# Kernel tuning notes

Hardware: AMD Instinct MI355X
Metric: run time of the kernel (lower is better)

## Reference

```python
import jax, jax.numpy as jnp
import numpy as np

B, L, HS = 2, 2048, 2048
NH, NKV, HD = 16, 4, 128
EPS = 1e-6
ROPE_BASE = 10000.0
SCALE = HD ** -0.5


def setup_inputs() -> dict:
    key = jax.random.key(0)
    ks = jax.random.split(key, 5)
    w = lambda k, shape: (jax.random.normal(k, shape, jnp.float32) * 0.02)
    return {
        "hidden_states": jax.random.normal(ks[0], (B, L, HS), jnp.float32),
        "Wq": w(ks[1], (HS, NH * HD)),
        "Wk": w(ks[2], (HS, NKV * HD)),
        "Wv": w(ks[3], (HS, NKV * HD)),
        "Wo": w(ks[4], (NH * HD, HS)),
        "q_norm_w": jnp.ones((HD,), jnp.float32),
        "k_norm_w": jnp.ones((HD,), jnp.float32),
    }


def _rmsnorm(x, w):
    return x * jax.lax.rsqrt(jnp.mean(x * x, axis=-1, keepdims=True) + EPS) * w


def _rope(x, cos, sin):
    # x: [B, L, heads, HD]; cos/sin: [1, L, 1, HD//2]
    x1, x2 = jnp.split(x, 2, axis=-1)
    return jnp.concatenate([x1 * cos - x2 * sin, x2 * cos + x1 * sin], axis=-1)


def reference(hidden_states, Wq, Wk, Wv, Wo, q_norm_w, k_norm_w):
    b, l, _ = hidden_states.shape
    n_rep = NH // NKV
    q = (hidden_states @ Wq).reshape(b, l, NH, HD)
    k = (hidden_states @ Wk).reshape(b, l, NKV, HD)
    v = (hidden_states @ Wv).reshape(b, l, NKV, HD)
    # QK RMSNorm over head_dim
    q = _rmsnorm(q, q_norm_w)
    k = _rmsnorm(k, k_norm_w)
    # RoPE with position_ids = arange(L)
    pos = jnp.arange(l, dtype=jnp.float32)
    inv_freq = 1.0 / (ROPE_BASE ** (jnp.arange(0, HD, 2, dtype=jnp.float32) / HD))
    ang = pos[:, None] * inv_freq  # [L, HD//2]
    cos = jnp.cos(ang)[None, :, None, :]
    sin = jnp.sin(ang)[None, :, None, :]
    q = _rope(q, cos, sin)
    k = _rope(k, cos, sin)
    # GQA: torch expand+reshape gives q head h -> kv head (h mod NKV);
    # reshape q to [B, L, n_rep, NKV, HD] (h = r*NKV + j) and contract per kv group.
    qg = q.reshape(b, l, n_rep, NKV, HD)
    scores = jnp.einsum("blrjd,bmjd->brjlm", qg, k) * SCALE  # [B, r, j, L, L]
    causal = jnp.tril(jnp.ones((l, l), dtype=bool))
    scores = jnp.where(causal, scores, -jnp.inf)
    probs = jax.nn.softmax(scores, axis=-1)
    out = jnp.einsum("brjlm,bmjd->blrjd", probs, v).reshape(b, l, NH * HD)
    return out @ Wo
```

## Files before the change

kernel.cpp:

```cpp
#include <hip/hip_runtime.h>
#include <hip/hip_bf16.h>

#define B_  2
#define L_  2048
#define HS_ 2048
#define NH_ 16
#define NKV_ 4
#define HD_ 128
#define EPS_ 1e-6f
#define SCALE_ 0.08838834764831843f
#define LOG2E_ 1.4426950408889634f

typedef __attribute__((ext_vector_type(8))) short bf16x8;
typedef __attribute__((ext_vector_type(4))) float f32x4;

__device__ __forceinline__ f32x4 mfma16(bf16x8 a, bf16x8 b, f32x4 c) {
    return __builtin_amdgcn_mfma_f32_16x16x32_bf16(a, b, c, 0, 0, 0);
}

__device__ __forceinline__ void async_copy16(void* lds, const void* g) {
    __builtin_amdgcn_global_load_lds(
        (const __attribute__((address_space(1))) unsigned int*)g,
        (__attribute__((address_space(3))) unsigned int*)lds,
        16, 0, 0);
}

__device__ __forceinline__ unsigned cvtpk(float lo, float hi) {
    unsigned r;
    asm("v_cvt_pk_bf16_f32 %0, %1, %2" : "=v"(r) : "v"(lo), "v"(hi));
    return r;
}

__global__ __launch_bounds__(256) void fused_prep(
    const float* __restrict__ hidden, __hip_bfloat16* __restrict__ A_h,
    const float* __restrict__ Wq, __hip_bfloat16* __restrict__ Wq_t,
    const float* __restrict__ Wk, __hip_bfloat16* __restrict__ Wk_t,
    const float* __restrict__ Wv, __hip_bfloat16* __restrict__ Wv_t,
    const float* __restrict__ Wo, __hip_bfloat16* __restrict__ Wo_t) {
    __shared__ float tile[32][33];
    int bid = blockIdx.x;
    if (bid < 8192) {
        int i = bid * 256 + threadIdx.x;
        float4 v = ((const float4*)hidden)[i];
        union { __hip_bfloat16 h[4]; short4 s; } u;
        u.h[0] = __float2bfloat16(v.x);
        u.h[1] = __float2bfloat16(v.y);
        u.h[2] = __float2bfloat16(v.z);
        u.h[3] = __float2bfloat16(v.w);
        ((short4*)A_h)[i] = u.s;
        return;
    }
    const float* src; __hip_bfloat16* dst; int N, tb;
    if (bid < 12288)      { tb = bid - 8192;  src = Wq; dst = Wq_t; N = 2048; }
    else if (bid < 13312) { tb = bid - 12288; src = Wk; dst = Wk_t; N = 512;  }
    else if (bid < 14336) { tb = bid - 13312; src = Wv; dst = Wv_t; N = 512;  }
    else                  { tb = bid - 14336; src = Wo; dst = Wo_t; N = 2048; }
    int nt = N >> 5;
    int n0 = (tb % nt) * 32, k0 = (tb / nt) * 32;
    int tx = threadIdx.x & 31, ty = threadIdx.x >> 5;
#pragma unroll
    for (int i = 0; i < 32; i += 8)
        tile[ty + i][tx] = src[(size_t)(k0 + ty + i) * N + n0 + tx];
    __syncthreads();
#pragma unroll
    for (int i = 0; i < 32; i += 8)
        dst[(size_t)(n0 + ty + i) * HS_ + k0 + tx] = __float2bfloat16(tile[tx][ty + i]);
}

__device__ __forceinline__ void norm_rope_row(const float* __restrict__ X,
                                              __hip_bfloat16* __restrict__ Y,
                                              const float* __restrict__ w,
                                              int row, int lane,
                                              int log2nh, int in_stride, float oscale) {
    int m = row >> log2nh;
    int head = row & ((1 << log2nh) - 1);
    int pos = m & (L_ - 1);
    const float* x = X + (size_t)m * in_stride + head * HD_;
    float x1 = x[lane], x2 = x[lane + 64];
    float ss = x1 * x1 + x2 * x2;
#pragma unroll
    for (int mm = 1; mm < 64; mm <<= 1) ss += __shfl_xor(ss, mm);
    float rms = rsqrtf(ss * (1.0f / 128.0f) + EPS_);
    float xn1 = x1 * rms * w[lane];
    float xn2 = x2 * rms * w[lane + 64];
    float inv_freq = __builtin_exp2f(-(float)lane * 0.20762050593046014f);
    float ang = (float)pos * inv_freq;
    float c = cosf(ang), s = sinf(ang);
    __hip_bfloat16* y = Y + (size_t)row * HD_;
    y[lane]      = __float2bfloat16((xn1 * c - xn2 * s) * oscale);
    y[lane + 64] = __float2bfloat16((xn2 * c + xn1 * s) * oscale);
}

__global__ __launch_bounds__(256) void fused_norm_v(
    const float* __restrict__ q_f32, __hip_bfloat16* __restrict__ q_bf,
    const float* __restrict__ kv_f32, __hip_bfloat16* __restrict__ k_bf,
    __hip_bfloat16* __restrict__ vt_bf,
    const float* __restrict__ qw, const float* __restrict__ kw) {
    __shared__ float tile[32][33];
    int bid = blockIdx.x;
    int lane = threadIdx.x & 63;
    if (bid < 16384) {
        int row = bid * 4 + (threadIdx.x >> 6);
        norm_rope_row(q_f32, q_bf, qw, row, lane, 4, 2048, SCALE_ * LOG2E_);
        return;
    }
    if (bid < 20480) {
        int row = (bid - 16384) * 4 + (threadIdx.x >> 6);
        norm_rope_row(kv_f32, k_bf, kw, row, lane, 2, 1024, 1.0f);
        return;
    }
    int vbid = bid - 20480;
    int xb = vbid & 63, yb = (vbid >> 6) & 3, zb = vbid >> 8;
    int b = zb >> 2, kv = zb & 3;
    int l0 = xb * 32, d0 = yb * 32;
    int tx = threadIdx.x & 31, ty = threadIdx.x >> 5;
#pragma unroll
    for (int i = 0; i < 32; i += 8)
        tile[ty + i][tx] = kv_f32[(size_t)(b * L_ + l0 + ty + i) * 1024 + 512 + kv * HD_ + d0 + tx];
    __syncthreads();
#pragma unroll
    for (int i = 0; i < 32; i += 8)
        vt_bf[((size_t)(b * NKV_ + kv) * HD_ + d0 + ty + i) * L_ + l0 + tx] =
            __float2bfloat16(tile[tx][ty + i]);
}

#define GNT 32
#define GKB 4096
__global__ __launch_bounds__(512, 2) void gemm8_bf16(const __hip_bfloat16* __restrict__ A,
                                                     const __hip_bfloat16* __restrict__ Bt,
                                                     float* __restrict__ C1,
                                                     float* __restrict__ C2,
                                                     int Ntot, int splitN) {
    __shared__ __align__(16) char lds[131072];
    int t = threadIdx.x;
    int w = t >> 6, lane = t & 63;
    int row16 = lane & 15, quad = lane >> 4, e7 = row16 & 7;
    int wr = w >> 2, wc = w & 3;

    int gx = gridDim.x;
    int nwg = gx * gridDim.y;
    int bid = blockIdx.y * gx + blockIdx.x;
    int cpx = nwg >> 3;
    int swz = (bid & 7) * cpx + (bid >> 3);
    int bx = swz % gx, by = swz / gx;
    int m0 = bx * 256, n0 = by * 256;

    const char* baseA[2];
    const char* baseB[2];
#pragma unroll
    for (int kc = 0; kc < 2; ++kc) {
        int so = ((kc * 4 + quad) ^ e7) << 4;
        baseA[kc] = lds + wr * 16384 + row16 * 128 + so;
        baseB[kc] = lds + 65536 + wc * 8192 + row16 * 128 + so;
    }

    int r8 = lane >> 3;
    int sl = (lane & 7) ^ r8;
    char* dstA = lds + wr * 16384 + (w & 3) * 2048 + lane * 16;
    char* dstB = lds + 65536 + (w >> 1) * 8192 + (w & 1) * 2048 + lane * 16;
    const char* gA = (const char*)A +
        (size_t)(m0 + wr * 128 + (w & 3) * 16 + r8) * GKB + sl * 16;
    const char* gB = (const char*)Bt +
        (size_t)(n0 + (w >> 1) * 64 + (w & 1) * 16 + r8) * GKB + sl * 16;

    f32x4 acc[8][4] = {};
    bf16x8 a[4][2], b[2][2];

#pragma unroll
    for (int i = 0; i < 2; ++i) async_copy16(dstA + i * 1024, gA + i * 32768);
#pragma unroll
    for (int i = 0; i < 2; ++i) async_copy16(dstB + i * 1024, gB + i * 32768);
#pragma unroll
    for (int i = 0; i < 2; ++i) async_copy16(dstB + 4096 + i * 1024, gB + 131072 + i * 32768);
#pragma unroll
    for (int i = 0; i < 2; ++i) async_copy16(dstA + 8192 + i * 1024, gA + 262144 + i * 32768);

    for (int Tb = 0; Tb < GNT; Tb += 2) {
#pragma unroll
        for (int u = 0; u < 2; ++u) {
            const int T = Tb + u;
            const int cu = u * 32768, du = (u ^ 1) * 32768;
            const int tn = (T + 1 < GNT ? T + 1 : T) * 128;

            asm volatile("s_waitcnt vmcnt(4)" ::: "memory");
            __builtin_amdgcn_s_barrier();
            __builtin_amdgcn_sched_barrier(0);
#pragma unroll
            for (int mi = 0; mi < 4; ++mi)
#pragma unroll
                for (int kc = 0; kc < 2; ++kc)
                    a[mi][kc] = *(const bf16x8*)(baseA[kc] + cu + mi * 2048);
#pragma unroll
            for (int ni = 0; ni < 2; ++ni)
#pragma unroll
                for (int kc = 0; kc < 2; ++kc)
                    b[ni][kc] = *(const bf16x8*)(baseB[kc] + cu + ni * 2048);
#pragma unroll
            for (int i = 0; i < 2; ++i)
                async_copy16(dstA + du + i * 1024, gA + tn + i * 32768);
            asm volatile("s_waitcnt lgkmcnt(0)" ::: "memory");
            __builtin_amdgcn_sched_barrier(0);
            __builtin_amdgcn_s_setprio(1);
#pragma unroll
            for (int mi = 0; mi < 4; ++mi)
#pragma unroll
                for (int ni = 0; ni < 2; ++ni)
#pragma unroll
                    for (int kc = 0; kc < 2; ++kc)
                        acc[mi][ni] = mfma16(a[mi][kc], b[ni][kc], acc[mi][ni]);
            __builtin_amdgcn_s_setprio(0);

            asm volatile("s_waitcnt vmcnt(4)" ::: "memory");
            __builtin_amdgcn_s_barrier();
            __builtin_amdgcn_sched_barrier(0);
#pragma unroll
            for (int ni = 0; ni < 2; ++ni)
#pragma unroll
                for (int kc = 0; kc < 2; ++kc)
                    b[ni][kc] = *(const bf16x8*)(baseB[kc] + cu + 4096 + ni * 2048);
#pragma unroll
            for (int i = 0; i < 2; ++i)
                async_copy16(dstB + du + i * 1024, gB + tn + i * 32768);
            asm volatile("s_waitcnt lgkmcnt(0)" ::: "memory");
            __builtin_amdgcn_sched_barrier(0);
            __builtin_amdgcn_s_setprio(1);
#pragma unroll
            for (int mi = 0; mi < 4; ++mi)
#pragma unroll
                for (int ni = 0; ni < 2; ++ni)
#pragma unroll
                    for (int kc = 0; kc < 2; ++kc)
                        acc[mi][2 + ni] = mfma16(a[mi][kc], b[ni][kc], acc[mi][2 + ni]);
            __builtin_amdgcn_s_setprio(0);

            asm volatile("s_waitcnt vmcnt(4)" ::: "memory");
            __builtin_amdgcn_s_barrier();
            __builtin_amdgcn_sched_barrier(0);
#pragma unroll
            for (int mi = 0; mi < 4; ++mi)
#pragma unroll
                for (int kc = 0; kc < 2; ++kc)
                    a[mi][kc] = *(const bf16x8*)(baseA[kc] + cu + 8192 + mi * 2048);
#pragma unroll
            for (int i = 0; i < 2; ++i)
                async_copy16(dstB + du + 4096 + i * 1024, gB + 131072 + tn + i * 32768);
            asm volatile("s_waitcnt lgkmcnt(0)" ::: "memory");
            __builtin_amdgcn_sched_barrier(0);
            __builtin_amdgcn_s_setprio(1);
#pragma unroll
            for (int mi = 0; mi < 4; ++mi)
#pragma unroll
                for (int ni = 0; ni < 2; ++ni)
#pragma unroll
                    for (int kc = 0; kc < 2; ++kc)
                        acc[4 + mi][2 + ni] = mfma16(a[mi][kc], b[ni][kc], acc[4 + mi][2 + ni]);
            __builtin_amdgcn_s_setprio(0);

            __builtin_amdgcn_s_barrier();
            __builtin_amdgcn_sched_barrier(0);
#pragma unroll
            for (int ni = 0; ni < 2; ++ni)
#pragma unroll
                for (int kc = 0; kc < 2; ++kc)
                    b[ni][kc] = *(const bf16x8*)(baseB[kc] + cu + ni * 2048);
#pragma unroll
            for (int i = 0; i < 2; ++i)
                async_copy16(dstA + du + 8192 + i * 1024, gA + 262144 + tn + i * 32768);
            asm volatile("s_waitcnt lgkmcnt(0)" ::: "memory");
            __builtin_amdgcn_sched_barrier(0);
            __builtin_amdgcn_s_setprio(1);
#pragma unroll
            for (int mi = 0; mi < 4; ++mi)
#pragma unroll
                for (int ni = 0; ni < 2; ++ni)
#pragma unroll
                    for (int kc = 0; kc < 2; ++kc)
                        acc[4 + mi][ni] = mfma16(a[mi][kc], b[ni][kc], acc[4 + mi][ni]);
            __builtin_amdgcn_s_setprio(0);
        }
    }

    float* Cb; int cs, ccol0;
    if (n0 < splitN) { Cb = C1; cs = splitN; ccol0 = n0; }
    else             { Cb = C2; cs = Ntot - splitN; ccol0 = n0 - splitN; }
#pragma unroll
    for (int mi = 0; mi < 8; ++mi)
#pragma unroll
        for (int ni = 0; ni < 4; ++ni) {
            int rbase = m0 + wr * 128 + mi * 16 + quad * 4;
            int col = ccol0 + wc * 64 + ni * 16 + row16;
#pragma unroll
            for (int r = 0; r < 4; ++r)
                Cb[(size_t)(rbase + r) * cs + col] = acc[mi][ni][r];
        }
}

__global__ __launch_bounds__(512, 2) void gemm_o(const __hip_bfloat16* __restrict__ A,
                                                 const __hip_bfloat16* __restrict__ Bt,
                                                 float* __restrict__ C) {
    __shared__ __align__(16) char lds[98304];
    int t = threadIdx.x;
    int w = t >> 6, lane = t & 63;
    int row16 = lane & 15, quad = lane >> 4, e7 = row16 & 15 & 7;
    int wr = w >> 2, wc = w & 3;

    int gx = gridDim.x;
    int nwg = gx * gridDim.y;
    int bid = blockIdx.y * gx + blockIdx.x;
    int cpx = nwg >> 3;
    int swz = (bid & 7) * cpx + (bid >> 3);
    int bx = swz % gx, by = swz / gx;
    int m0 = bx * 128, n0 = by * 256;

    const char* baseA[2];
    const char* baseB[2];
#pragma unroll
    for (int kc = 0; kc < 2; ++kc) {
        int so = ((kc * 4 + quad) ^ e7) << 4;
        baseA[kc] = lds + wr * 8192 + row16 * 128 + so;
        baseB[kc] = lds + 32768 + wc * 8192 + row16 * 128 + so;
    }

    int r8 = lane >> 3;
    int sl = (lane & 7) ^ r8;
    int arow_lo = ((w & 4) << 4) + (w & 3) * 8;
    int li0 = w * 2;
    int brow_lo0 = ((li0) >> 2) * 64 + ((li0) & 3) * 8;
    int brow_lo1 = ((li0 + 1) >> 2) * 64 + ((li0 + 1) & 3) * 8;

    char* dAlo = lds + arow_lo * 128 + lane * 16;
    char* dBlo0 = lds + 32768 + brow_lo0 * 128 + lane * 16;
    char* dBlo1 = lds + 32768 + brow_lo1 * 128 + lane * 16;
    const char* gAlo = (const char*)A + (size_t)(m0 + arow_lo + r8) * GKB + sl * 16;
    const char* gBlo0 = (const char*)Bt + (size_t)(n0 + brow_lo0 + r8) * GKB + sl * 16;
    const char* gBlo1 = (const char*)Bt + (size_t)(n0 + brow_lo1 + r8) * GKB + sl * 16;
    const int HI_L = 32 * 128;
    const size_t HI_G = (size_t)32 * GKB;

    f32x4 acc[4][4] = {};
    bf16x8 a[2][2], b[2][2];

    async_copy16(dAlo, gAlo);
    async_copy16(dBlo0, gBlo0);
    async_copy16(dBlo1, gBlo1);
    async_copy16(dBlo0 + HI_L, gBlo0 + HI_G);
    async_copy16(dBlo1 + HI_L, gBlo1 + HI_G);
    async_copy16(dAlo + HI_L, gAlo + HI_G);

    for (int Tb = 0; Tb < GNT; Tb += 2) {
#pragma unroll
        for (int u = 0; u < 2; ++u) {
            const int T = Tb + u;
            const int cuA = u * 16384, duA = (u ^ 1) * 16384;
            const int cuB = u * 32768, duB = (u ^ 1) * 32768;
            const int tn = (T + 1 < GNT ? T + 1 : T) * 128;

            asm volatile("s_waitcnt vmcnt(3)" ::: "memory");
            __builtin_amdgcn_s_barrier();
            __builtin_amdgcn_sched_barrier(0);
#pragma unroll
            for (int mi = 0; mi < 2; ++mi)
#pragma unroll
                for (int kc = 0; kc < 2; ++kc)
                    a[mi][kc] = *(const bf16x8*)(baseA[kc] + cuA + mi * 2048);
#pragma unroll
            for (int ni = 0; ni < 2; ++ni)
#pragma unroll
                for (int kc = 0; kc < 2; ++kc)
                    b[ni][kc] = *(const bf16x8*)(baseB[kc] + cuB + ni * 2048);
            async_copy16(dAlo + duA, gAlo + tn);
            asm volatile("s_waitcnt lgkmcnt(0)" ::: "memory");
            __builtin_amdgcn_sched_barrier(0);
            __builtin_amdgcn_s_setprio(1);
#pragma unroll
            for (int mi = 0; mi < 2; ++mi)
#pragma unroll
                for (int ni = 0; ni < 2; ++ni)
#pragma unroll
                    for (int kc = 0; kc < 2; ++kc)
                        acc[mi][ni] = mfma16(a[mi][kc], b[ni][kc], acc[mi][ni]);
            __builtin_amdgcn_s_setprio(0);

            asm volatile("s_waitcnt vmcnt(2)" ::: "memory");
            __builtin_amdgcn_s_barrier();
            __builtin_amdgcn_sched_barrier(0);
#pragma unroll
            for (int ni = 0; ni < 2; ++ni)
#pragma unroll
                for (int kc = 0; kc < 2; ++kc)
                    b[ni][kc] = *(const bf16x8*)(baseB[kc] + cuB + 4096 + ni * 2048);
            async_copy16(dBlo0 + duB, gBlo0 + tn);
            async_copy16(dBlo1 + duB, gBlo1 + tn);
            asm volatile("s_waitcnt lgkmcnt(0)" ::: "memory");
            __builtin_amdgcn_sched_barrier(0);
            __builtin_amdgcn_s_setprio(1);
#pragma unroll
            for (int mi = 0; mi < 2; ++mi)
#pragma unroll
                for (int ni = 0; ni < 2; ++ni)
#pragma unroll
                    for (int kc = 0; kc < 2; ++kc)
                        acc[mi][2 + ni] = mfma16(a[mi][kc], b[ni][kc], acc[mi][2 + ni]);
            __builtin_amdgcn_s_setprio(0);

            asm volatile("s_waitcnt vmcnt(3)" ::: "memory");
            __builtin_amdgcn_s_barrier();
            __builtin_amdgcn_sched_barrier(0);
#pragma unroll
            for (int mi = 0; mi < 2; ++mi)
#pragma unroll
                for (int kc = 0; kc < 2; ++kc)
                    a[mi][kc] = *(const bf16x8*)(baseA[kc] + cuA + 4096 + mi * 2048);
            async_copy16(dBlo0 + HI_L + duB, gBlo0 + HI_G + tn);
            async_copy16(dBlo1 + HI_L + duB, gBlo1 + HI_G + tn);
            asm volatile("s_waitcnt lgkmcnt(0)" ::: "memory");
            __builtin_amdgcn_sched_barrier(0);
            __builtin_amdgcn_s_setprio(1);
#pragma unroll
            for (int mi = 0; mi < 2; ++mi)
#pragma unroll
                for (int ni = 0; ni < 2; ++ni)
#pragma unroll
                    for (int kc = 0; kc < 2; ++kc)
                        acc[2 + mi][2 + ni] = mfma16(a[mi][kc], b[ni][kc], acc[2 + mi][2 + ni]);
            __builtin_amdgcn_s_setprio(0);

            __builtin_amdgcn_s_barrier();
            __builtin_amdgcn_sched_barrier(0);
#pragma unroll
            for (int ni = 0; ni < 2; ++ni)
#pragma unroll
                for (int kc = 0; kc < 2; ++kc)
                    b[ni][kc] = *(const bf16x8*)(baseB[kc] + cuB + ni * 2048);
            async_copy16(dAlo + HI_L + duA, gAlo + HI_G + tn);
            asm volatile("s_waitcnt lgkmcnt(0)" ::: "memory");
            __builtin_amdgcn_sched_barrier(0);
            __builtin_amdgcn_s_setprio(1);
#pragma unroll
            for (int mi = 0; mi < 2; ++mi)
#pragma unroll
                for (int ni = 0; ni < 2; ++ni)
#pragma unroll
                    for (int kc = 0; kc < 2; ++kc)
                        acc[2 + mi][ni] = mfma16(a[mi][kc], b[ni][kc], acc[2 + mi][ni]);
            __builtin_amdgcn_s_setprio(0);
        }
    }
    asm volatile("s_waitcnt vmcnt(0)" ::: "memory");

#pragma unroll
    for (int mi = 0; mi < 4; ++mi)
#pragma unroll
        for (int ni = 0; ni < 4; ++ni) {
            int rbase = m0 + wr * 64 + mi * 16 + quad * 4;
            int col = n0 + wc * 64 + ni * 16 + row16;
#pragma unroll
            for (int r = 0; r < 4; ++r)
                C[(size_t)(rbase + r) * 2048 + col] = acc[mi][ni][r];
        }
}

__global__ __launch_bounds__(256, 2) void flash_attn(const __hip_bfloat16* __restrict__ Q,
                                                     const __hip_bfloat16* __restrict__ Kb,
                                                     const __hip_bfloat16* __restrict__ Vt,
                                                     __hip_bfloat16* __restrict__ O) {
    __shared__ __align__(16) __hip_bfloat16 sK[2][64 * 128];
    __shared__ __align__(16) __hip_bfloat16 sV[2][128 * 64];
    __shared__ __align__(16) __hip_bfloat16 sP[4][16 * 72];

    int t = threadIdx.x, wave = t >> 6, lane = t & 63;
    int row16 = lane & 15, quad = lane >> 4;
    int h = blockIdx.y, b = blockIdx.z;
    int kv = h & (NKV_ - 1);
    int x = blockIdx.x;
    int qtA = x, qtB = 31 - x;
    int nA = qtA + 1;
    const int nTot = 33;

    int e7 = row16 & 7;
    int kOff[4], vOff[2];
#pragma unroll
    for (int kc = 0; kc < 4; ++kc)
        kOff[kc] = row16 * 256 + (((kc * 4 + quad) ^ e7) * 16);
#pragma unroll
    for (int kc2 = 0; kc2 < 2; ++kc2)
        vOff[kc2] = row16 * 128 + (((kc2 * 4 + quad) ^ e7) * 16);

    const char* sKb = (const char*)&sK[0][0];
    const char* sVb = (const char*)&sV[0][0];
    char* myP = (char*)&sP[wave][0];
    int pW = row16 * 144 + quad * 8;
    int pR = row16 * 144 + quad * 16;

    const char* gK[4];
    const char* gV[4];
#pragma unroll
    for (int i = 0; i < 4; ++i) {
        int rk = wave * 16 + i * 4 + quad;
        int ck = row16 ^ (rk & 7);
        gK[i] = (const char*)(Kb + ((size_t)(b * L_ + rk) * NKV_ + kv) * HD_ + ck * 8);
        int rv = wave * 32 + i * 8 + (lane >> 3);
        int cv = (lane & 7) ^ (rv & 7);
        gV[i] = (const char*)(Vt + ((size_t)(b * NKV_ + kv) * HD_ + rv) * L_ + cv * 8);
    }
    char* dK = (char*)&sK[0][0] + wave * 4096 + lane * 16;
    char* dV = (char*)&sV[0][0] + wave * 4096 + lane * 16;

    bf16x8 qf[4];
    f32x4 accO[8];
    float lrow;
    int q0w = 0;

    auto loadQ = [&](int qt) {
        q0w = qt * 64 + wave * 16;
        const __hip_bfloat16* qbase =
            Q + ((size_t)(b * L_ + q0w + row16) * NH_ + h) * HD_ + quad * 8;
#pragma unroll
        for (int kc = 0; kc < 4; ++kc) qf[kc] = *(const bf16x8*)(qbase + kc * 32);
#pragma unroll
        for (int db = 0; db < 8; ++db) accO[db] = f32x4{0.f, 0.f, 0.f, 0.f};
        lrow = 0.f;
    };

    auto epilogue = [&]() {
        float l = lrow;
        l += __shfl_xor(l, 16);
        l += __shfl_xor(l, 32);
        float linv = 1.0f / l;
        __hip_bfloat16* obase = O + ((size_t)(b * L_ + q0w + row16) * NH_ + h) * HD_;
#pragma unroll
        for (int db = 0; db < 8; ++db) {
            union { __hip_bfloat16 h4[4]; short4 s4; } u;
#pragma unroll
            for (int r = 0; r < 4; ++r) u.h4[r] = __float2bfloat16(accO[db][r] * linv);
            *(short4*)(obase + db * 16 + quad * 4) = u.s4;
        }
    };

    auto stage = [&](int s1) {
        int kb64 = (s1 < nA ? s1 : s1 - nA) * 64;
        int buf = (s1 & 1) * 16384;
        int ko = kb64 * 1024;
        int vo = kb64 * 2;
#pragma unroll
        for (int i = 0; i < 4; ++i) {
            async_copy16(dK + buf + i * 1024, gK[i] + ko);
            async_copy16(dV + buf + i * 1024, gV[i] + vo);
        }
    };

    loadQ(qtA);
    stage(0);
    for (int s = 0; s < nTot; ++s) {
        __syncthreads();
        if (s + 1 < nTot) stage(s + 1);
        if (s == nA) { epilogue(); loadQ(qtB); }
        int kcur = (s < nA ? s : s - nA) * 64;
        const char* cK = sKb + (s & 1) * 16384;
        const char* cV = sVb + (s & 1) * 16384;

        f32x4 st[4];
        __builtin_amdgcn_s_setprio(1);
#pragma unroll
        for (int kb = 0; kb < 4; ++kb) {
            f32x4 acc = {};
#pragma unroll
            for (int kc = 0; kc < 4; ++kc) {
                bf16x8 kf = *(const bf16x8*)(cK + kb * 4096 + kOff[kc]);
                acc = mfma16(kf, qf[kc], acc);
            }
            st[kb] = acc;
        }
        __builtin_amdgcn_s_setprio(0);

        float p[4][4];
        if (kcur + 63 > q0w) {
            int qgRel = q0w + row16 - kcur - quad * 4;
#pragma unroll
            for (int kb = 0; kb < 4; ++kb)
#pragma unroll
                for (int r = 0; r < 4; ++r) {
                    float e = __builtin_exp2f(st[kb][r]);
                    p[kb][r] = (kb * 16 + r <= qgRel) ? e : 0.f;
                }
        } else {
#pragma unroll
            for (int kb = 0; kb < 4; ++kb)
#pragma unroll
                for (int r = 0; r < 4; ++r)
                    p[kb][r] = __builtin_exp2f(st[kb][r]);
        }
#pragma unroll
        for (int kb = 0; kb < 4; ++kb)
#pragma unroll
            for (int r = 0; r < 4; ++r) lrow += p[kb][r];

#pragma unroll
        for (int kb = 0; kb < 4; ++kb) {
            uint2 u;
            u.x = cvtpk(p[kb][0], p[kb][1]);
            u.y = cvtpk(p[kb][2], p[kb][3]);
            *(uint2*)(myP + pW + kb * 32) = u;
        }
        asm volatile("s_waitcnt lgkmcnt(0)" ::: "memory");
        bf16x8 pf[2];
        pf[0] = *(const bf16x8*)(myP + pR);
        pf[1] = *(const bf16x8*)(myP + pR + 64);

        __builtin_amdgcn_s_setprio(1);
#pragma unroll
        for (int db = 0; db < 8; ++db) {
#pragma unroll
            for (int kc2 = 0; kc2 < 2; ++kc2) {
                bf16x8 vf = *(const bf16x8*)(cV + db * 2048 + vOff[kc2]);
                accO[db] = mfma16(vf, pf[kc2], accO[db]);
            }
        }
        __builtin_amdgcn_s_setprio(0);
    }
    epilogue();
}

extern "C" void kernel_launch(void* const* d_in, const int* in_sizes, int n_in,
                              void* d_out, int out_size, void* d_ws, size_t ws_size,
                              hipStream_t stream) {
    const float* hidden = (const float*)d_in[0];
    const float* Wq = (const float*)d_in[1];
    const float* Wk = (const float*)d_in[2];
    const float* Wv = (const float*)d_in[3];
    const float* Wo = (const float*)d_in[4];
    const float* qw = (const float*)d_in[5];
    const float* kw = (const float*)d_in[6];
    float* out = (float*)d_out;

    char* ws = (char*)d_ws;
    size_t off = 0;
    auto alloc = [&](size_t bytes) { char* p = ws + off; off += (bytes + 255) & ~255ull; return p; };
    __hip_bfloat16* Wq_t = (__hip_bfloat16*)alloc((size_t)HS_ * NH_ * HD_ * 2);
    __hip_bfloat16* Wk_t = (__hip_bfloat16*)alloc((size_t)HS_ * NKV_ * HD_ * 2);
    __hip_bfloat16* Wv_t = (__hip_bfloat16*)alloc((size_t)HS_ * NKV_ * HD_ * 2);
    __hip_bfloat16* Wo_t = (__hip_bfloat16*)alloc((size_t)HS_ * NH_ * HD_ * 2);
    __hip_bfloat16* A_h  = (__hip_bfloat16*)alloc((size_t)B_ * L_ * HS_ * 2);
    float* kv_f32 = (float*)alloc((size_t)B_ * L_ * 1024 * 4);
    __hip_bfloat16* q_bf  = (__hip_bfloat16*)alloc((size_t)B_ * L_ * NH_ * HD_ * 2);
    __hip_bfloat16* k_bf  = (__hip_bfloat16*)alloc((size_t)B_ * L_ * NKV_ * HD_ * 2);
    __hip_bfloat16* vt_bf = (__hip_bfloat16*)alloc((size_t)B_ * NKV_ * HD_ * L_ * 2);
    float* q_f32 = out;
    __hip_bfloat16* attn_bf = A_h;

    const int M = B_ * L_;

    fused_prep<<<18432, 256, 0, stream>>>(hidden, A_h, Wq, Wq_t, Wk, Wk_t, Wv, Wv_t, Wo, Wo_t);
    gemm8_bf16<<<dim3(M / 256, 3072 / 256), 512, 0, stream>>>(
        A_h, Wq_t, q_f32, kv_f32, 3072, 2048);
    fused_norm_v<<<22528, 256, 0, stream>>>(q_f32, q_bf, kv_f32, k_bf, vt_bf, qw, kw);
    flash_attn<<<dim3(16, NH_, B_), 256, 0, stream>>>(q_bf, k_bf, vt_bf, attn_bf);
    gemm_o<<<dim3(M / 128, 2048 / 256), 512, 0, stream>>>(attn_bf, Wo_t, out);
}
```

Baseline: 291.5 us.

## Restructure flash attention to 2-wave blocks with 32-row KV tiles and per-wave Q reuse

The attention kernel moves from 4-wave blocks that each process a paired (qtA, 31-qtA) tile set to 2-wave blocks that each own one 64-row query tile. Inside a block, each wave now handles 32 query rows as two 16-row groups, so every K and V fragment read from LDS feeds two MFMAs. KV tiles shrink to 32 rows, which halves LDS use, and the grid doubles to 1024 blocks, interleaving low and high tiles to balance causal work. The aim is more LDS-to-MFMA reuse and finer-grained scheduling, at the cost of more barrier steps per block and higher register pressure from the doubled accumulators.

```diff
diff --git a/kernel.cpp b/kernel.cpp
--- a/kernel.cpp
+++ b/kernel.cpp
@@ -460,165 +460,179 @@
         }
 }
 
-__global__ __launch_bounds__(256, 2) void flash_attn(const __hip_bfloat16* __restrict__ Q,
+__global__ __launch_bounds__(128, 2) void flash_attn(const __hip_bfloat16* __restrict__ Q,
                                                      const __hip_bfloat16* __restrict__ Kb,
                                                      const __hip_bfloat16* __restrict__ Vt,
                                                      __hip_bfloat16* __restrict__ O) {
-    __shared__ __align__(16) __hip_bfloat16 sK[2][64 * 128];
-    __shared__ __align__(16) __hip_bfloat16 sV[2][128 * 64];
-    __shared__ __align__(16) __hip_bfloat16 sP[4][16 * 72];
+    __shared__ __align__(16) __hip_bfloat16 sK[2][32 * 128];
+    __shared__ __align__(16) __hip_bfloat16 sV[2][128 * 32];
+    __shared__ __align__(16) __hip_bfloat16 sP[2][16 * 40];
 
     int t = threadIdx.x, wave = t >> 6, lane = t & 63;
     int row16 = lane & 15, quad = lane >> 4;
     int h = blockIdx.y, b = blockIdx.z;
     int kv = h & (NKV_ - 1);
-    int x = blockIdx.x;
-    int qtA = x, qtB = 31 - x;
-    int nA = qtA + 1;
-    const int nTot = 33;
+    int u = blockIdx.x;
+    int qt = (u & 1) ? 31 - (u >> 1) : (u >> 1);
+    int nSteps = 2 * qt + 2;
 
     int e7 = row16 & 7;
-    int kOff[4], vOff[2];
+    int kOff[4];
 #pragma unroll
     for (int kc = 0; kc < 4; ++kc)
         kOff[kc] = row16 * 256 + (((kc * 4 + quad) ^ e7) * 16);
-#pragma unroll
-    for (int kc2 = 0; kc2 < 2; ++kc2)
-        vOff[kc2] = row16 * 128 + (((kc2 * 4 + quad) ^ e7) * 16);
+    int vOff = row16 * 64 + ((quad ^ (row16 & 3)) * 16);
 
     const char* sKb = (const char*)&sK[0][0];
     const char* sVb = (const char*)&sV[0][0];
     char* myP = (char*)&sP[wave][0];
-    int pW = row16 * 144 + quad * 8;
-    int pR = row16 * 144 + quad * 16;
+    int pW = row16 * 80 + quad * 8;
+    int pR = row16 * 80 + quad * 16;
 
     const char* gK[4];
     const char* gV[4];
 #pragma unroll
     for (int i = 0; i < 4; ++i) {
-        int rk = wave * 16 + i * 4 + quad;
-        int ck = row16 ^ (rk & 7);
+        int rk = i * 8 + (lane >> 4);
+        rk = i * 8 + (t >> 4);
+        int ck = (t & 15) ^ (rk & 7);
         gK[i] = (const char*)(Kb + ((size_t)(b * L_ + rk) * NKV_ + kv) * HD_ + ck * 8);
-        int rv = wave * 32 + i * 8 + (lane >> 3);
-        int cv = (lane & 7) ^ (rv & 7);
+        int rv = i * 32 + (t >> 2);
+        int cv = (t & 3) ^ (rv & 3);
         gV[i] = (const char*)(Vt + ((size_t)(b * NKV_ + kv) * HD_ + rv) * L_ + cv * 8);
     }
-    char* dK = (char*)&sK[0][0] + wave * 4096 + lane * 16;
-    char* dV = (char*)&sV[0][0] + wave * 4096 + lane * 16;
-
-    bf16x8 qf[4];
-    f32x4 accO[8];
-    float lrow;
-    int q0w = 0;
-
-    auto loadQ = [&](int qt) {
-        q0w = qt * 64 + wave * 16;
+    char* dK = (char*)&sK[0][0] + t * 16;
+    char* dV = (char*)&sV[0][0] + t * 16;
+
+    int q0w = qt * 64 + wave * 32;
+
+    bf16x8 qf[2][4];
+    f32x4 accO[2][8];
+    float lrow[2];
+#pragma unroll
+    for (int qg = 0; qg < 2; ++qg) {
         const __hip_bfloat16* qbase =
-            Q + ((size_t)(b * L_ + q0w + row16) * NH_ + h) * HD_ + quad * 8;
-#pragma unroll
-        for (int kc = 0; kc < 4; ++kc) qf[kc] = *(const bf16x8*)(qbase + kc * 32);
-#pragma unroll
-        for (int db = 0; db < 8; ++db) accO[db] = f32x4{0.f, 0.f, 0.f, 0.f};
-        lrow = 0.f;
+            Q + ((size_t)(b * L_ + q0w + qg * 16 + row16) * NH_ + h) * HD_ + quad * 8;
+#pragma unroll
+        for (int kc = 0; kc < 4; ++kc) qf[qg][kc] = *(const bf16x8*)(qbase + kc * 32);
+#pragma unroll
+        for (int db = 0; db < 8; ++db) accO[qg][db] = f32x4{0.f, 0.f, 0.f, 0.f};
+        lrow[qg] = 0.f;
+    }
+
+    auto stage = [&](int s1) {
+        int buf = (s1 & 1) * 8192;
+        int ko = s1 * 32768;
+        int vo = s1 * 64;
+#pragma unroll
+        for (int i = 0; i < 4; ++i) {
+            async_copy16(dK + buf + i * 2048, gK[i] + ko);
+            async_copy16(dV + buf + i * 2048, gV[i] + vo);
+        }
     };
 
-    auto epilogue = [&]() {
-        float l = lrow;
+    stage(0);
+    for (int s = 0; s < nSteps; ++s) {
+        __syncthreads();
+        if (s + 1 < nSteps) stage(s + 1);
+        int kcur = s * 32;
+        const char* cK = sKb + (s & 1) * 8192;
+        const char* cV = sVb + (s & 1) * 8192;
+
+        f32x4 st[2][2];
+        __builtin_amdgcn_s_setprio(1);
+#pragma unroll
+        for (int kb = 0; kb < 2; ++kb) {
+            bf16x8 kf[4];
+#pragma unroll
+            for (int kc = 0; kc < 4; ++kc)
+                kf[kc] = *(const bf16x8*)(cK + kb * 4096 + kOff[kc]);
+#pragma unroll
+            for (int qg = 0; qg < 2; ++qg) {
+                f32x4 acc = {};
+#pragma unroll
+                for (int kc = 0; kc < 4; ++kc)
+                    acc = mfma16(kf[kc], qf[qg][kc], acc);
+                st[qg][kb] = acc;
+            }
+        }
+        __builtin_amdgcn_s_setprio(0);
+
+        float p[2][2][4];
+        if (kcur + 31 > q0w) {
+#pragma unroll
+            for (int qg = 0; qg < 2; ++qg) {
+                int qgRel = q0w + qg * 16 + row16 - kcur - quad * 4;
+#pragma unroll
+                for (int kb = 0; kb < 2; ++kb)
+#pragma unroll
+                    for (int r = 0; r < 4; ++r) {
+                        float e = __builtin_exp2f(st[qg][kb][r]);
+                        p[qg][kb][r] = (kb * 16 + r <= qgRel) ? e : 0.f;
+                    }
+            }
+        } else {
+#pragma unroll
+            for (int qg = 0; qg < 2; ++qg)
+#pragma unroll
+                for (int kb = 0; kb < 2; ++kb)
+#pragma unroll
+                    for (int r = 0; r < 4; ++r)
+                        p[qg][kb][r] = __builtin_exp2f(st[qg][kb][r]);
+        }
+#pragma unroll
+        for (int qg = 0; qg < 2; ++qg)
+#pragma unroll
+            for (int kb = 0; kb < 2; ++kb)
+#pragma unroll
+                for (int r = 0; r < 4; ++r) lrow[qg] += p[qg][kb][r];
+
+        bf16x8 pf0, pf1;
+#pragma unroll
+        for (int kb = 0; kb < 2; ++kb) {
+            uint2 uu;
+            uu.x = cvtpk(p[0][kb][0], p[0][kb][1]);
+            uu.y = cvtpk(p[0][kb][2], p[0][kb][3]);
+            *(uint2*)(myP + pW + kb * 32) = uu;
+        }
+        asm volatile("s_waitcnt lgkmcnt(0)" ::: "memory");
+        pf0 = *(const bf16x8*)(myP + pR);
+#pragma unroll
+        for (int kb = 0; kb < 2; ++kb) {
+            uint2 uu;
+            uu.x = cvtpk(p[1][kb][0], p[1][kb][1]);
+            uu.y = cvtpk(p[1][kb][2], p[1][kb][3]);
+            *(uint2*)(myP + pW + kb * 32) = uu;
+        }
+        asm volatile("s_waitcnt lgkmcnt(0)" ::: "memory");
+        pf1 = *(const bf16x8*)(myP + pR);
+
+        __builtin_amdgcn_s_setprio(1);
+#pragma unroll
+        for (int db = 0; db < 8; ++db) {
+            bf16x8 vf = *(const bf16x8*)(cV + db * 1024 + vOff);
+            accO[0][db] = mfma16(vf, pf0, accO[0][db]);
+            accO[1][db] = mfma16(vf, pf1, accO[1][db]);
+        }
+        __builtin_amdgcn_s_setprio(0);
+    }
+
+#pragma unroll
+    for (int qg = 0; qg < 2; ++qg) {
+        float l = lrow[qg];
         l += __shfl_xor(l, 16);
         l += __shfl_xor(l, 32);
         float linv = 1.0f / l;
-        __hip_bfloat16* obase = O + ((size_t)(b * L_ + q0w + row16) * NH_ + h) * HD_;
+        __hip_bfloat16* obase =
+            O + ((size_t)(b * L_ + q0w + qg * 16 + row16) * NH_ + h) * HD_;
 #pragma unroll
         for (int db = 0; db < 8; ++db) {
-            union { __hip_bfloat16 h4[4]; short4 s4; } u;
-#pragma unroll
-            for (int r = 0; r < 4; ++r) u.h4[r] = __float2bfloat16(accO[db][r] * linv);
-            *(short4*)(obase + db * 16 + quad * 4) = u.s4;
-        }
-    };
-
-    auto stage = [&](int s1) {
-        int kb64 = (s1 < nA ? s1 : s1 - nA) * 64;
-        int buf = (s1 & 1) * 16384;
-        int ko = kb64 * 1024;
-        int vo = kb64 * 2;
-#pragma unroll
-        for (int i = 0; i < 4; ++i) {
-            async_copy16(dK + buf + i * 1024, gK[i] + ko);
-            async_copy16(dV + buf + i * 1024, gV[i] + vo);
-        }
-    };
-
-    loadQ(qtA);
-    stage(0);
-    for (int s = 0; s < nTot; ++s) {
-        __syncthreads();
-        if (s + 1 < nTot) stage(s + 1);
-        if (s == nA) { epilogue(); loadQ(qtB); }
-        int kcur = (s < nA ? s : s - nA) * 64;
-        const char* cK = sKb + (s & 1) * 16384;
-        const char* cV = sVb + (s & 1) * 16384;
-
-        f32x4 st[4];
-        __builtin_amdgcn_s_setprio(1);
-#pragma unroll
-        for (int kb = 0; kb < 4; ++kb) {
-            f32x4 acc = {};
-#pragma unroll
-            for (int kc = 0; kc < 4; ++kc) {
-                bf16x8 kf = *(const bf16x8*)(cK + kb * 4096 + kOff[kc]);
-                acc = mfma16(kf, qf[kc], acc);
-            }
-            st[kb] = acc;
-        }
-        __builtin_amdgcn_s_setprio(0);
-
-        float p[4][4];
-        if (kcur + 63 > q0w) {
-            int qgRel = q0w + row16 - kcur - quad * 4;
-#pragma unroll
-            for (int kb = 0; kb < 4; ++kb)
-#pragma unroll
-                for (int r = 0; r < 4; ++r) {
-                    float e = __builtin_exp2f(st[kb][r]);
-                    p[kb][r] = (kb * 16 + r <= qgRel) ? e : 0.f;
-                }
-        } else {
-#pragma unroll
-            for (int kb = 0; kb < 4; ++kb)
-#pragma unroll
-                for (int r = 0; r < 4; ++r)
-                    p[kb][r] = __builtin_exp2f(st[kb][r]);
-        }
-#pragma unroll
-        for (int kb = 0; kb < 4; ++kb)
-#pragma unroll
-            for (int r = 0; r < 4; ++r) lrow += p[kb][r];
-
-#pragma unroll
-        for (int kb = 0; kb < 4; ++kb) {
-            uint2 u;
-            u.x = cvtpk(p[kb][0], p[kb][1]);
-            u.y = cvtpk(p[kb][2], p[kb][3]);
-            *(uint2*)(myP + pW + kb * 32) = u;
-        }
-        asm volatile("s_waitcnt lgkmcnt(0)" ::: "memory");
-        bf16x8 pf[2];
-        pf[0] = *(const bf16x8*)(myP + pR);
-        pf[1] = *(const bf16x8*)(myP + pR + 64);
-
-        __builtin_amdgcn_s_setprio(1);
-#pragma unroll
-        for (int db = 0; db < 8; ++db) {
-#pragma unroll
-            for (int kc2 = 0; kc2 < 2; ++kc2) {
-                bf16x8 vf = *(const bf16x8*)(cV + db * 2048 + vOff[kc2]);
-                accO[db] = mfma16(vf, pf[kc2], accO[db]);
-            }
-        }
-        __builtin_amdgcn_s_setprio(0);
-    }
-    epilogue();
+            union { __hip_bfloat16 h4[4]; short4 s4; } uo;
+#pragma unroll
+            for (int r = 0; r < 4; ++r) uo.h4[r] = __float2bfloat16(accO[qg][db][r] * linv);
+            *(short4*)(obase + db * 16 + quad * 4) = uo.s4;
+        }
+    }
 }
 
 extern "C" void kernel_launch(void* const* d_in, const int* in_sizes, int n_in,
@@ -654,6 +668,6 @@
     gemm8_bf16<<<dim3(M / 256, 3072 / 256), 512, 0, stream>>>(
         A_h, Wq_t, q_f32, kv_f32, 3072, 2048);
     fused_norm_v<<<22528, 256, 0, stream>>>(q_f32, q_bf, kv_f32, k_bf, vt_bf, qw, kw);
-    flash_attn<<<dim3(16, NH_, B_), 256, 0, stream>>>(q_bf, k_bf, vt_bf, attn_bf);
+    flash_attn<<<dim3(32, NH_, B_), 128, 0, stream>>>(q_bf, k_bf, vt_bf, attn_bf);
     gemm_o<<<dim3(M / 128, 2048 / 256), 512, 0, stream>>>(attn_bf, Wo_t, out);
 }
```

Measured after the change: 323.5 us. 11.0% more time.
